# Kernel optimization log

Hardware: AMD Instinct MI355X
Metric: run time of the kernel (lower is better)

Reference implementation:

```python
import jax, jax.numpy as jnp
import numpy as np

D_MODEL = 1024
NUM_HEADS = 16
HEAD_DIM = D_MODEL // NUM_HEADS
D_FF = 4096
THETA = 10000.0
MAX_SEQ_LEN = 2048
EPS = 1e-5


def _init_linear(key, out_f, in_f):
    std = np.sqrt(2.0 / (out_f + in_f))
    w = jax.random.truncated_normal(key, -3.0, 3.0, (out_f, in_f), dtype=jnp.float32) * std
    return w


def setup_inputs() -> dict:
    key = jax.random.key(0)
    ks = jax.random.split(key, 9)
    x = jax.random.normal(ks[0], (4, 2048, D_MODEL), dtype=jnp.float32)
    return {
        "x": x,
        "wq": _init_linear(ks[1], D_MODEL, D_MODEL),
        "wk": _init_linear(ks[2], D_MODEL, D_MODEL),
        "wv": _init_linear(ks[3], D_MODEL, D_MODEL),
        "wo": _init_linear(ks[4], D_MODEL, D_MODEL),
        "ln1_w": jnp.ones((D_MODEL,), jnp.float32),
        "ln2_w": jnp.ones((D_MODEL,), jnp.float32),
        "up_w": _init_linear(ks[5], D_FF, D_MODEL),
        "gate_w": _init_linear(ks[6], D_FF, D_MODEL),
        "down_w": _init_linear(ks[7], D_MODEL, D_FF),
    }


def _rmsnorm(x, w):
    xf = x.astype(jnp.float32)
    inv_rms = jax.lax.rsqrt(jnp.mean(xf * xf, axis=-1, keepdims=True) + EPS)
    return (xf * inv_rms * w).astype(x.dtype)


def _rope_tables(seq_len):
    inv_freq = 1.0 / THETA ** (jnp.arange(0, HEAD_DIM, 2, dtype=jnp.float32) / HEAD_DIM)
    t = jnp.arange(seq_len, dtype=jnp.float32)
    freqs = jnp.outer(t, inv_freq)  # [s, hd/2]
    return jnp.cos(freqs), jnp.sin(freqs)


def _apply_rope(x, cos, sin):
    # x: [b, h, s, hd]; cos/sin: [s, hd/2] -> broadcast over b,h
    xe = x[..., 0::2]
    xo = x[..., 1::2]
    oe = xe * cos - xo * sin
    oo = xo * cos + xe * sin
    return jnp.stack((oe, oo), axis=-1).reshape(x.shape)


def reference(x, wq, wk, wv, wo, ln1_w, ln2_w, up_w, gate_w, down_w):
    b, s, d = x.shape
    h, hd = NUM_HEADS, HEAD_DIM

    # --- attention sublayer (pre-norm) ---
    xn = _rmsnorm(x, ln1_w)
    q = (xn @ wq.T).reshape(b, s, h, hd).transpose(0, 2, 1, 3)
    k = (xn @ wk.T).reshape(b, s, h, hd).transpose(0, 2, 1, 3)
    v = (xn @ wv.T).reshape(b, s, h, hd).transpose(0, 2, 1, 3)

    cos, sin = _rope_tables(s)
    q = _apply_rope(q, cos, sin)
    k = _apply_rope(k, cos, sin)

    scale = 1.0 / jnp.sqrt(jnp.float32(hd))
    logits = jnp.einsum("bhqd,bhkd->bhqk", q, k)
    causal = jnp.tril(jnp.ones((s, s), dtype=bool))
    logits = jnp.where(causal, logits, -jnp.inf)
    attn = jax.nn.softmax(logits * scale, axis=-1)
    ao = jnp.einsum("bhqk,bhkd->bhqd", attn, v)
    ao = ao.transpose(0, 2, 1, 3).reshape(b, s, d) @ wo.T
    x = x + ao

    # --- SwiGLU FFN sublayer (pre-norm) ---
    xn = _rmsnorm(x, ln2_w)
    up = xn @ up_w.T
    gate = xn @ gate_w.T
    ff = (up * jax.nn.sigmoid(up) * gate) @ down_w.T
    return x + ff
```

## Files before the change

### kernel.cpp

```cpp
#include <hip/hip_runtime.h>
#include <stdint.h>

#define SEQ   2048
#define NTOK  8192

typedef unsigned short u16;
typedef __bf16 bf16x8 __attribute__((ext_vector_type(8)));
typedef float  f32x4  __attribute__((ext_vector_type(4)));
typedef float  f32x16 __attribute__((ext_vector_type(16)));

__device__ __forceinline__ float b2f(u16 b) {
    union { unsigned u; float f; } v; v.u = ((unsigned)b) << 16; return v.f;
}
__device__ __forceinline__ u16 f2b(float f) {
    union { float f; unsigned u; } v; v.f = f;
    unsigned r = (v.u + 0x7fffu + ((v.u >> 16) & 1u)) >> 16;
    return (u16)r;
}
__device__ __forceinline__ u16 f2b_trunc(float f) {
    union { float f; unsigned u; } v; v.f = f;
    return (u16)(v.u >> 16);
}

__device__ __forceinline__ void gl_lds16(const void* g, void* l) {
    __builtin_amdgcn_global_load_lds(
        (const __attribute__((address_space(1))) void*)g,
        (__attribute__((address_space(3))) void*)l,
        16, 0, 0);
}

__global__ __launch_bounds__(256)
void cvt_all(const float* __restrict__ wq, const float* __restrict__ wk,
             const float* __restrict__ wv, const float* __restrict__ wo,
             const float* __restrict__ wup, const float* __restrict__ wgt,
             const float* __restrict__ wdn,
             u16* __restrict__ dq, u16* __restrict__ dk, u16* __restrict__ dv,
             u16* __restrict__ dw, u16* __restrict__ du, u16* __restrict__ dg,
             u16* __restrict__ dd)
{
    const int bid = blockIdx.x;
    const float* s; u16* d; int off;
    if (bid < 4096) {
        const int which = bid >> 10;
        off = (bid & 1023) * 256 + threadIdx.x;
        s = which == 0 ? wq : which == 1 ? wk : which == 2 ? wv : wo;
        d = which == 0 ? dq : which == 1 ? dk : which == 2 ? dv : dw;
    } else {
        const int which = (bid - 4096) >> 12;
        off = ((bid - 4096) & 4095) * 256 + threadIdx.x;
        s = which == 0 ? wup : which == 1 ? wgt : wdn;
        d = which == 0 ? du  : which == 1 ? dg  : dd;
    }
    float4 v = ((const float4*)s)[off];
    ushort4 o;
    o.x = f2b(v.x); o.y = f2b(v.y); o.z = f2b(v.z); o.w = f2b(v.w);
    ((ushort4*)d)[off] = o;
}

template<int EPI>
__global__ __launch_bounds__(256)
void gemm_bt(const u16* __restrict__ A, const u16* __restrict__ B,
             void* __restrict__ C, const void* __restrict__ E,
             int M, int N, int K, int ldc, int coff)
{
    __shared__ __align__(16) u16 As[128 * 64];
    __shared__ __align__(16) u16 Bs[128 * 64];

    const int tid  = threadIdx.x;
    const int lane = tid & 63;
    const int wid  = tid >> 6;
    const int m0 = blockIdx.y * 128;
    const int n0 = blockIdx.x * 128;
    const int wm = (wid >> 1) * 64;
    const int wn = (wid & 1) * 64;
    const int l31 = lane & 31, kg = lane >> 5;

    f32x16 acc[2][2];
#pragma unroll
    for (int i = 0; i < 2; i++)
#pragma unroll
        for (int j = 0; j < 2; j++)
#pragma unroll
            for (int r = 0; r < 16; r++) acc[i][j][r] = 0.f;

    const u16* Ag[4]; const u16* Bg[4]; u16* Al[4]; u16* Bl[4];
#pragma unroll
    for (int j = 0; j < 4; j++) {
        const int q = j * 256 + tid;
        const int r = q >> 3, s = q & 7, c = s ^ (r & 7);
        Ag[j] = A + (size_t)(m0 + r) * K + c * 8;
        Bg[j] = B + (size_t)(n0 + r) * K + c * 8;
        Al[j] = As + q * 8;
        Bl[j] = Bs + q * 8;
    }

    int arow[2], brow[2];
#pragma unroll
    for (int i = 0; i < 2; i++) { arow[i] = wm + i * 32 + l31; }
#pragma unroll
    for (int j = 0; j < 2; j++) { brow[j] = wn + j * 32 + l31; }

    for (int kt = 0; kt < K; kt += 64) {
        __syncthreads();
#pragma unroll
        for (int j = 0; j < 4; j++) {
            gl_lds16(Ag[j] + kt, Al[j]);
            gl_lds16(Bg[j] + kt, Bl[j]);
        }
        __syncthreads();

#pragma unroll
        for (int s = 0; s < 4; s++) {
            const int ch = s * 2 + kg;
            bf16x8 af[2], bf[2];
#pragma unroll
            for (int i = 0; i < 2; i++)
                af[i] = *(const bf16x8*)(
                    &As[arow[i] * 64 + ((ch ^ (arow[i] & 7)) * 8)]);
#pragma unroll
            for (int j = 0; j < 2; j++)
                bf[j] = *(const bf16x8*)(
                    &Bs[brow[j] * 64 + ((ch ^ (brow[j] & 7)) * 8)]);
#pragma unroll
            for (int i = 0; i < 2; i++)
#pragma unroll
                for (int j = 0; j < 2; j++)
                    acc[i][j] = __builtin_amdgcn_mfma_f32_32x32x16_bf16(
                        af[i], bf[j], acc[i][j], 0, 0, 0);
        }
    }

#pragma unroll
    for (int i = 0; i < 2; i++) {
#pragma unroll
        for (int r = 0; r < 16; r++) {
            const int row = m0 + wm + i * 32 + (r & 3) + 8 * (r >> 2) + 4 * kg;
#pragma unroll
            for (int j = 0; j < 2; j++) {
                const int col = n0 + wn + j * 32 + l31;
                const size_t idx = (size_t)row * ldc + coff + col;
                const float v = acc[i][j][r];
                if (EPI == 0) {
                    ((u16*)C)[idx] = f2b(v);
                } else {
                    ((float*)C)[idx] = v + ((const float*)E)[idx];
                }
            }
        }
    }
}

__global__ __launch_bounds__(256)
void gemm_mlp(const u16* __restrict__ A, const u16* __restrict__ Bg,
              const u16* __restrict__ Bu, u16* __restrict__ C, int K)
{
    __shared__ __align__(16) u16 As[128 * 64];
    __shared__ __align__(16) u16 Gs[64 * 64];
    __shared__ __align__(16) u16 Us[64 * 64];

    const int tid  = threadIdx.x;
    const int lane = tid & 63;
    const int wid  = tid >> 6;
    const int m0 = blockIdx.y * 128;
    const int n0 = blockIdx.x * 64;
    const int wm = (wid >> 1) * 64;
    const int wn = (wid & 1) * 32;
    const int l31 = lane & 31, kg = lane >> 5;

    f32x16 ag[2], au[2];
#pragma unroll
    for (int i = 0; i < 2; i++)
#pragma unroll
        for (int r = 0; r < 16; r++) { ag[i][r] = 0.f; au[i][r] = 0.f; }

    const u16* Ag[4]; u16* Al[4];
#pragma unroll
    for (int j = 0; j < 4; j++) {
        const int q = j * 256 + tid;
        const int r = q >> 3, s = q & 7, c = s ^ (r & 7);
        Ag[j] = A + (size_t)(m0 + r) * K + c * 8;
        Al[j] = As + q * 8;
    }
    const u16* Gg[2]; const u16* Ug[2]; u16* Gl[2]; u16* Ul[2];
#pragma unroll
    for (int j = 0; j < 2; j++) {
        const int q = j * 256 + tid;
        const int r = q >> 3, s = q & 7, c = s ^ (r & 7);
        Gg[j] = Bg + (size_t)(n0 + r) * K + c * 8;
        Ug[j] = Bu + (size_t)(n0 + r) * K + c * 8;
        Gl[j] = Gs + q * 8;
        Ul[j] = Us + q * 8;
    }

    int arow[2];
#pragma unroll
    for (int i = 0; i < 2; i++) arow[i] = wm + i * 32 + l31;
    const int brow = wn + l31;

    for (int kt = 0; kt < K; kt += 64) {
        __syncthreads();
#pragma unroll
        for (int j = 0; j < 4; j++) gl_lds16(Ag[j] + kt, Al[j]);
#pragma unroll
        for (int j = 0; j < 2; j++) {
            gl_lds16(Gg[j] + kt, Gl[j]);
            gl_lds16(Ug[j] + kt, Ul[j]);
        }
        __syncthreads();

#pragma unroll
        for (int s = 0; s < 4; s++) {
            const int ch = s * 2 + kg;
            bf16x8 af[2], gf, uf;
#pragma unroll
            for (int i = 0; i < 2; i++)
                af[i] = *(const bf16x8*)(
                    &As[arow[i] * 64 + ((ch ^ (arow[i] & 7)) * 8)]);
            gf = *(const bf16x8*)(&Gs[brow * 64 + ((ch ^ (brow & 7)) * 8)]);
            uf = *(const bf16x8*)(&Us[brow * 64 + ((ch ^ (brow & 7)) * 8)]);
#pragma unroll
            for (int i = 0; i < 2; i++) {
                ag[i] = __builtin_amdgcn_mfma_f32_32x32x16_bf16(
                    af[i], gf, ag[i], 0, 0, 0);
                au[i] = __builtin_amdgcn_mfma_f32_32x32x16_bf16(
                    af[i], uf, au[i], 0, 0, 0);
            }
        }
    }

#pragma unroll
    for (int i = 0; i < 2; i++) {
#pragma unroll
        for (int r = 0; r < 16; r++) {
            const int row = m0 + wm + i * 32 + (r & 3) + 8 * (r >> 2) + 4 * kg;
            const int col = n0 + wn + l31;
            const float u = au[i][r];
            const float g = ag[i][r];
            C[(size_t)row * 4096 + col] = f2b(u / (1.f + __expf(-u)) * g);
        }
    }
}

__global__ __launch_bounds__(256)
void rmsnorm_k(const float* __restrict__ xin, const float* __restrict__ w,
               u16* __restrict__ o)
{
    const int t = blockIdx.x;
    const int tid = threadIdx.x;
    float4 xv = ((const float4*)xin)[(size_t)t * 256 + tid];
    float ss = xv.x * xv.x + xv.y * xv.y + xv.z * xv.z + xv.w * xv.w;
#pragma unroll
    for (int off = 32; off > 0; off >>= 1) ss += __shfl_down(ss, off);
    __shared__ float red[4];
    const int lane = tid & 63, wv_ = tid >> 6;
    if (lane == 0) red[wv_] = ss;
    __syncthreads();
    const float tot = red[0] + red[1] + red[2] + red[3];
    const float inv = rsqrtf(tot * (1.f / 1024.f) + 1e-5f);
    float4 ww = ((const float4*)w)[tid];
    ushort4 ov;
    ov.x = f2b(xv.x * inv * ww.x);
    ov.y = f2b(xv.y * inv * ww.y);
    ov.z = f2b(xv.z * inv * ww.z);
    ov.w = f2b(xv.w * inv * ww.w);
    ((ushort4*)o)[(size_t)t * 256 + tid] = ov;
}

#define QSCALE 0.18033688011112042f

__global__ void rope_tab(float* __restrict__ cs, float* __restrict__ sn)
{
    const int s = blockIdx.x;
    const int i = threadIdx.x;
    const double inv = exp(-((double)(2 * i) / 64.0) * log(10000.0));
    const double ang = (double)s * inv;
    cs[s * 32 + i] = (float)cos(ang);
    sn[s * 32 + i] = (float)sin(ang);
}

__global__ __launch_bounds__(256)
void rope_apply(u16* __restrict__ qkv, const float* __restrict__ cs,
                const float* __restrict__ sn)
{
    const int t = blockIdx.x;
    const int s = t & (SEQ - 1);
    u16* row = qkv + (size_t)t * 3072;
    __shared__ float c_s[32], s_s[32];
    if (threadIdx.x < 32) {
        c_s[threadIdx.x] = cs[s * 32 + threadIdx.x];
        s_s[threadIdx.x] = sn[s * 32 + threadIdx.x];
    }
    __syncthreads();
#pragma unroll
    for (int rr = 0; rr < 2; rr++) {
        const int item = rr * 256 + threadIdx.x;
        const int hh = item >> 5, i = item & 31;
        const int f = hh * 64 + 2 * i;
        const float c = c_s[i], sv = s_s[i];
        float xe = b2f(row[f]), xo = b2f(row[f + 1]);
        row[f]     = f2b((xe * c - xo * sv) * QSCALE);
        row[f + 1] = f2b((xo * c + xe * sv) * QSCALE);
        xe = b2f(row[1024 + f]); xo = b2f(row[1024 + f + 1]);
        row[1024 + f]     = f2b(xe * c - xo * sv);
        row[1024 + f + 1] = f2b(xo * c + xe * sv);
    }
}

__global__ __launch_bounds__(256)
void vtrans(const u16* __restrict__ qkv, u16* __restrict__ vt)
{
    __shared__ u16 Ld[64 * 264];
    const int bh = blockIdx.x, st = blockIdx.y;
    const int b = bh >> 4, h = bh & 15;
    const int tid = threadIdx.x;
    const u16* src = qkv + ((size_t)(b * SEQ + st * 256 + tid)) * 3072 + 2048 + h * 64;
    uint4 v[8];
#pragma unroll
    for (int c = 0; c < 8; c++) v[c] = *(const uint4*)(src + c * 8);
#pragma unroll
    for (int c = 0; c < 8; c++) {
        const u16* pv = (const u16*)&v[c];
#pragma unroll
        for (int j = 0; j < 8; j++)
            Ld[(c * 8 + j) * 264 + tid] = pv[j];
    }
    __syncthreads();
    u16* dst = vt + (size_t)bh * (64 * SEQ) + st * 256;
#pragma unroll
    for (int cc = 0; cc < 8; cc++) {
        const int c = cc * 256 + tid;
        const int d = c >> 5, t8 = (c & 31) * 8;
        *(uint4*)(dst + (size_t)d * SEQ + t8) = *(const uint4*)(&Ld[d * 264 + t8]);
    }
}

__global__ __launch_bounds__(512)
void attn(const u16* __restrict__ qkv, const u16* __restrict__ vt,
          u16* __restrict__ ao)
{
    __shared__ __align__(16) u16 Ks[64 * 72];
    __shared__ __align__(16) u16 Vt[64 * 72];
    __shared__ __align__(16) u16 Ps[8][16 * 72];

    const int bh = blockIdx.x;
    const int qy = blockIdx.y;
    const int b = bh >> 4, h = bh & 15;
    const int tid = threadIdx.x, lane = tid & 63, wid = tid >> 6;
    const int am = lane & 15, grp = lane >> 4;
    const size_t tok0 = (size_t)b * SEQ;
    const u16* qbase = qkv + tok0 * 3072 + h * 64;
    const u16* kbase = qbase + 1024;
    const u16* vtg = vt + (size_t)bh * (64 * SEQ);

    union { uint4 u; bf16x8 b; } onesu;
    onesu.u = (uint4){0x3f803f80u, 0x3f803f80u, 0x3f803f80u, 0x3f803f80u};
    const bf16x8 ones = onesu.b;

    const int srow = tid >> 3, sc8 = (tid & 7) * 8;

#pragma unroll
    for (int tile = 0; tile < 2; tile++) {
        const int yt = tile == 0 ? qy : 15 - qy;
        const int qrow0 = yt * 128 + wid * 16;

        bf16x8 qf[2];
        {
            const u16* qp = qbase + (size_t)(qrow0 + am) * 3072 + grp * 8;
            qf[0] = *(const bf16x8*)(qp);
            qf[1] = *(const bf16x8*)(qp + 32);
        }

        f32x4 O[4], Ol;
#pragma unroll
        for (int j = 0; j < 4; j++) O[j] = (f32x4){0.f, 0.f, 0.f, 0.f};
        Ol = (f32x4){0.f, 0.f, 0.f, 0.f};

        const int ktend = yt * 128 + 64;
        for (int kt = 0; kt <= ktend; kt += 64) {
            __syncthreads();
            *(uint4*)(&Ks[srow * 72 + sc8]) =
                *(const uint4*)(kbase + (size_t)(kt + srow) * 3072 + sc8);
            *(uint4*)(&Vt[srow * 72 + sc8]) =
                *(const uint4*)(vtg + (size_t)srow * SEQ + kt + sc8);
            __syncthreads();

            if (kt > qrow0 + 15) continue;

            f32x4 st[4];
#pragma unroll
            for (int kk = 0; kk < 4; kk++) {
                const u16* kb = &Ks[(kk * 16 + am) * 72 + grp * 8];
                bf16x8 k0 = *(const bf16x8*)(kb);
                bf16x8 k1 = *(const bf16x8*)(kb + 32);
                f32x4 s = (f32x4){0.f, 0.f, 0.f, 0.f};
                s = __builtin_amdgcn_mfma_f32_16x16x32_bf16(qf[0], k0, s, 0, 0, 0);
                s = __builtin_amdgcn_mfma_f32_16x16x32_bf16(qf[1], k1, s, 0, 0, 0);
                st[kk] = s;
            }
            if (kt + 63 > qrow0) {
#pragma unroll
                for (int kk = 0; kk < 4; kk++) {
                    const int kg2 = kt + kk * 16 + am;
#pragma unroll
                    for (int r = 0; r < 4; r++) {
                        const int qg = qrow0 + grp * 4 + r;
                        if (kg2 > qg) st[kk][r] = -1e30f;
                    }
                }
            }
#pragma unroll
            for (int kk = 0; kk < 4; kk++)
#pragma unroll
                for (int r = 0; r < 4; r++)
                    st[kk][r] = exp2f(st[kk][r]);

            u16* pw = &Ps[wid][0];
#pragma unroll
            for (int kk = 0; kk < 4; kk++)
#pragma unroll
                for (int r = 0; r < 4; r++)
                    pw[(grp * 4 + r) * 72 + kk * 16 + am] = f2b_trunc(st[kk][r]);
            asm volatile("s_waitcnt lgkmcnt(0)" ::: "memory");

#pragma unroll
            for (int hh = 0; hh < 2; hh++) {
                bf16x8 pf = *(const bf16x8*)(&pw[am * 72 + hh * 32 + grp * 8]);
                Ol = __builtin_amdgcn_mfma_f32_16x16x32_bf16(pf, ones, Ol, 0, 0, 0);
#pragma unroll
                for (int jt = 0; jt < 4; jt++) {
                    bf16x8 vf = *(const bf16x8*)(
                        &Vt[(jt * 16 + am) * 72 + hh * 32 + grp * 8]);
                    O[jt] = __builtin_amdgcn_mfma_f32_16x16x32_bf16(
                        pf, vf, O[jt], 0, 0, 0);
                }
            }
        }

        u16* aorow = ao + (tok0 + qrow0) * 1024 + h * 64;
#pragma unroll
        for (int r = 0; r < 4; r++) {
            const int q = grp * 4 + r;
            const float invl = 1.f / Ol[r];
#pragma unroll
            for (int jt = 0; jt < 4; jt++)
                aorow[(size_t)q * 1024 + jt * 16 + am] = f2b(O[jt][r] * invl);
        }
    }
}

extern "C" void kernel_launch(void* const* d_in, const int* in_sizes, int n_in,
                              void* d_out, int out_size, void* d_ws, size_t ws_size,
                              hipStream_t stream)
{
    (void)in_sizes; (void)n_in; (void)out_size; (void)ws_size;
    const float* x     = (const float*)d_in[0];
    const float* wq    = (const float*)d_in[1];
    const float* wk    = (const float*)d_in[2];
    const float* wv    = (const float*)d_in[3];
    const float* wo    = (const float*)d_in[4];
    const float* ln1   = (const float*)d_in[5];
    const float* ln2   = (const float*)d_in[6];
    const float* wup   = (const float*)d_in[7];
    const float* wgate = (const float*)d_in[8];
    const float* wdown = (const float*)d_in[9];
    float* out = (float*)d_out;
    char* ws = (char*)d_ws;
    const size_t MB = 1024 * 1024;

    u16*   xn   = (u16*)(ws);
    u16*   ao   = (u16*)(ws);
    u16*   qkv  = (u16*)(ws + 16 * MB);
    u16*   hbuf = (u16*)(ws + 16 * MB);
    u16*   vtb  = (u16*)(ws + 64 * MB);
    float* x1   = (float*)(ws + 80 * MB);
    u16*   bwq  = (u16*)(ws + 112 * MB);
    u16*   bwk  = (u16*)(ws + 114 * MB);
    u16*   bwv  = (u16*)(ws + 116 * MB);
    u16*   bwo  = (u16*)(ws + 118 * MB);
    u16*   bwup = (u16*)(ws + 120 * MB);
    u16*   bwgt = (u16*)(ws + 128 * MB);
    u16*   bwdn = (u16*)(ws + 136 * MB);
    float* cst  = (float*)(ws + 144 * MB);
    float* snt  = (float*)(ws + 144 * MB + 262144);

    cvt_all<<<16384, 256, 0, stream>>>(wq, wk, wv, wo, wup, wgate, wdown,
                                       bwq, bwk, bwv, bwo, bwup, bwgt, bwdn);

    rope_tab<<<SEQ, 32, 0, stream>>>(cst, snt);
    rmsnorm_k<<<NTOK, 256, 0, stream>>>(x, ln1, xn);
    gemm_bt<0><<<dim3(24, 64), 256, 0, stream>>>(xn, bwq, qkv, nullptr, NTOK, 3072, 1024, 3072, 0);
    rope_apply<<<NTOK, 256, 0, stream>>>(qkv, cst, snt);
    vtrans<<<dim3(64, 8), 256, 0, stream>>>(qkv, vtb);
    attn<<<dim3(64, 8), 512, 0, stream>>>(qkv, vtb, ao);
    gemm_bt<1><<<dim3(8, 64), 256, 0, stream>>>(ao, bwo, x1, x, NTOK, 1024, 1024, 1024, 0);
    rmsnorm_k<<<NTOK, 256, 0, stream>>>(x1, ln2, xn);
    gemm_mlp<<<dim3(64, 64), 256, 0, stream>>>(xn, bwgt, bwup, hbuf, 1024);
    gemm_bt<1><<<dim3(8, 64), 256, 0, stream>>>(hbuf, bwdn, out, x1, NTOK, 1024, 4096, 1024, 0);
}
```

Baseline: 570.4 us.

## Rewrite gate/up MLP GEMM as 256x256 8-wave pipelined kernel with interleaved weights

Measured after the change: 565.8 us. No clear change (-0.8%).

```diff
diff --git a/kernel.cpp b/kernel.cpp
--- a/kernel.cpp
+++ b/kernel.cpp
@@ -35,26 +35,32 @@
              const float* __restrict__ wup, const float* __restrict__ wgt,
              const float* __restrict__ wdn,
              u16* __restrict__ dq, u16* __restrict__ dk, u16* __restrict__ dv,
-             u16* __restrict__ dw, u16* __restrict__ du, u16* __restrict__ dg,
-             u16* __restrict__ dd)
+             u16* __restrict__ dw, u16* __restrict__ dmu, u16* __restrict__ dd)
 {
     const int bid = blockIdx.x;
-    const float* s; u16* d; int off;
+    const float* s; u16* d; int osrc, odst;
     if (bid < 4096) {
         const int which = bid >> 10;
-        off = (bid & 1023) * 256 + threadIdx.x;
+        osrc = odst = (bid & 1023) * 256 + threadIdx.x;
         s = which == 0 ? wq : which == 1 ? wk : which == 2 ? wv : wo;
         d = which == 0 ? dq : which == 1 ? dk : which == 2 ? dv : dw;
     } else {
         const int which = (bid - 4096) >> 12;
-        off = ((bid - 4096) & 4095) * 256 + threadIdx.x;
-        s = which == 0 ? wup : which == 1 ? wgt : wdn;
-        d = which == 0 ? du  : which == 1 ? dg  : dd;
-    }
-    float4 v = ((const float4*)s)[off];
-    ushort4 o;
-    o.x = f2b(v.x); o.y = f2b(v.y); o.z = f2b(v.z); o.w = f2b(v.w);
-    ((ushort4*)d)[off] = o;
+        const int o = ((bid - 4096) & 4095) * 256 + threadIdx.x;
+        osrc = o;
+        if (which == 2) { s = wdn; d = dd; odst = o; }
+        else {
+            s = which == 0 ? wup : wgt;
+            d = dmu;
+            const int row = o >> 8;
+            const int rowp = ((row >> 4) << 5) + (row & 15) + (which == 0 ? 16 : 0);
+            odst = rowp * 256 + (o & 255);
+        }
+    }
+    float4 v = ((const float4*)s)[osrc];
+    ushort4 ov;
+    ov.x = f2b(v.x); ov.y = f2b(v.y); ov.z = f2b(v.z); ov.w = f2b(v.w);
+    ((ushort4*)d)[odst] = ov;
 }
 
 template<int EPI>
@@ -150,93 +156,158 @@
     }
 }
 
-__global__ __launch_bounds__(256)
-void gemm_mlp(const u16* __restrict__ A, const u16* __restrict__ Bg,
-              const u16* __restrict__ Bu, u16* __restrict__ C, int K)
-{
-    __shared__ __align__(16) u16 As[128 * 64];
-    __shared__ __align__(16) u16 Gs[64 * 64];
-    __shared__ __align__(16) u16 Us[64 * 64];
-
-    const int tid  = threadIdx.x;
-    const int lane = tid & 63;
-    const int wid  = tid >> 6;
-    const int m0 = blockIdx.y * 128;
-    const int n0 = blockIdx.x * 64;
-    const int wm = (wid >> 1) * 64;
-    const int wn = (wid & 1) * 32;
-    const int l31 = lane & 31, kg = lane >> 5;
-
-    f32x16 ag[2], au[2];
-#pragma unroll
-    for (int i = 0; i < 2; i++)
-#pragma unroll
-        for (int r = 0; r < 16; r++) { ag[i][r] = 0.f; au[i][r] = 0.f; }
-
-    const u16* Ag[4]; u16* Al[4];
-#pragma unroll
-    for (int j = 0; j < 4; j++) {
-        const int q = j * 256 + tid;
-        const int r = q >> 3, s = q & 7, c = s ^ (r & 7);
-        Ag[j] = A + (size_t)(m0 + r) * K + c * 8;
-        Al[j] = As + q * 8;
-    }
-    const u16* Gg[2]; const u16* Ug[2]; u16* Gl[2]; u16* Ul[2];
-#pragma unroll
-    for (int j = 0; j < 2; j++) {
-        const int q = j * 256 + tid;
-        const int r = q >> 3, s = q & 7, c = s ^ (r & 7);
-        Gg[j] = Bg + (size_t)(n0 + r) * K + c * 8;
-        Ug[j] = Bu + (size_t)(n0 + r) * K + c * 8;
-        Gl[j] = Gs + q * 8;
-        Ul[j] = Us + q * 8;
-    }
-
-    int arow[2];
-#pragma unroll
-    for (int i = 0; i < 2; i++) arow[i] = wm + i * 32 + l31;
-    const int brow = wn + l31;
-
-    for (int kt = 0; kt < K; kt += 64) {
-        __syncthreads();
-#pragma unroll
-        for (int j = 0; j < 4; j++) gl_lds16(Ag[j] + kt, Al[j]);
-#pragma unroll
-        for (int j = 0; j < 2; j++) {
-            gl_lds16(Gg[j] + kt, Gl[j]);
-            gl_lds16(Ug[j] + kt, Ul[j]);
-        }
-        __syncthreads();
-
-#pragma unroll
-        for (int s = 0; s < 4; s++) {
-            const int ch = s * 2 + kg;
-            bf16x8 af[2], gf, uf;
-#pragma unroll
-            for (int i = 0; i < 2; i++)
-                af[i] = *(const bf16x8*)(
-                    &As[arow[i] * 64 + ((ch ^ (arow[i] & 7)) * 8)]);
-            gf = *(const bf16x8*)(&Gs[brow * 64 + ((ch ^ (brow & 7)) * 8)]);
-            uf = *(const bf16x8*)(&Us[brow * 64 + ((ch ^ (brow & 7)) * 8)]);
-#pragma unroll
-            for (int i = 0; i < 2; i++) {
-                ag[i] = __builtin_amdgcn_mfma_f32_32x32x16_bf16(
-                    af[i], gf, ag[i], 0, 0, 0);
-                au[i] = __builtin_amdgcn_mfma_f32_32x32x16_bf16(
-                    af[i], uf, au[i], 0, 0, 0);
+#define MIDBAR \
+    __builtin_amdgcn_s_barrier(); \
+    asm volatile("s_waitcnt lgkmcnt(0)" ::: "memory"); \
+    __builtin_amdgcn_sched_barrier(0);
+
+#define PBAR \
+    __builtin_amdgcn_s_barrier(); \
+    asm volatile("" ::: "memory"); \
+    __builtin_amdgcn_sched_barrier(0);
+
+#define VMBAR4 \
+    asm volatile("s_waitcnt vmcnt(4)" ::: "memory"); \
+    __builtin_amdgcn_s_barrier(); \
+    asm volatile("" ::: "memory"); \
+    __builtin_amdgcn_sched_barrier(0);
+
+#define VMBAR0 \
+    asm volatile("s_waitcnt vmcnt(0)" ::: "memory"); \
+    __builtin_amdgcn_s_barrier(); \
+    asm volatile("" ::: "memory"); \
+    __builtin_amdgcn_sched_barrier(0);
+
+#define LDA(bufi, mh) { \
+    const u16* _ab = Ab##bufi + (mh) * 4096; \
+    _Pragma("unroll") \
+    for (int _m = 0; _m < 4; ++_m) { \
+        Aq[_m][0] = *(const bf16x8*)(_ab + _m * 1024 + axor0); \
+        Aq[_m][1] = *(const bf16x8*)(_ab + _m * 1024 + axor1); \
+    } }
+
+#define LDB(bufi, nh) { \
+    const u16* _bb = Bb##bufi + (nh) * 2048; \
+    _Pragma("unroll") \
+    for (int _n = 0; _n < 2; ++_n) { \
+        Bq[nh][_n][0] = *(const bf16x8*)(_bb + _n * 1024 + axor0); \
+        Bq[nh][_n][1] = *(const bf16x8*)(_bb + _n * 1024 + axor1); \
+    } }
+
+#define MM(mh, nh) \
+    __builtin_amdgcn_s_setprio(1); \
+    { _Pragma("unroll") \
+      for (int _m = 0; _m < 4; ++_m) { \
+        _Pragma("unroll") \
+        for (int _n = 0; _n < 2; ++_n) { \
+            acc[(mh)*4+_m][(nh)*2+_n] = __builtin_amdgcn_mfma_f32_16x16x32_bf16( \
+                Aq[_m][0], Bq[nh][_n][0], acc[(mh)*4+_m][(nh)*2+_n], 0, 0, 0); \
+            acc[(mh)*4+_m][(nh)*2+_n] = __builtin_amdgcn_mfma_f32_16x16x32_bf16( \
+                Aq[_m][1], Bq[nh][_n][1], acc[(mh)*4+_m][(nh)*2+_n], 0, 0, 0); \
+        } } } \
+    __builtin_amdgcn_s_setprio(0);
+
+#define STAGE_A(tile, half) { \
+    const u16* _s = pA0 + (size_t)(half) * 131072 + (size_t)(tile) * 64; \
+    u16* _d = lA0 + ((tile) & 1) * 16384 + (half) * 8192; \
+    gl_lds16(_s, _d); \
+    gl_lds16(_s + 65536, _d + 4096); }
+
+#define STAGE_B(tile, half) { \
+    const u16* _s = pB0 + (size_t)(half) * 131072 + (size_t)(tile) * 64; \
+    u16* _d = lB0 + ((tile) & 1) * 16384 + (half) * 8192; \
+    gl_lds16(_s, _d); \
+    gl_lds16(_s + 65536, _d + 4096); }
+
+__global__ __launch_bounds__(512, 2)
+void gemm8_mlp(const u16* __restrict__ A, const u16* __restrict__ Bc,
+               u16* __restrict__ H)
+{
+    __shared__ __align__(16) u16 As[32768];
+    __shared__ __align__(16) u16 Bs[32768];
+
+    const int tid = threadIdx.x, lane = tid & 63, wid = tid >> 6;
+    const int wr = wid >> 2, wc = wid & 3;
+    const int r15 = lane & 15, ks = lane >> 4;
+    const int m0 = blockIdx.y * 256, n0 = blockIdx.x * 256;
+
+    const int axor0 = ((ks) ^ (r15 & 7)) * 8;
+    const int axor1 = ((4 + ks) ^ (r15 & 7)) * 8;
+    const u16* Ab0 = As + wr * 8192 + r15 * 64;
+    const u16* Ab1 = As + 16384 + wr * 8192 + r15 * 64;
+    const u16* Bb0 = Bs + (wc >> 1) * 8192 + (wc & 1) * 4096 + r15 * 64;
+    const u16* Bb1 = Bs + 16384 + (wc >> 1) * 8192 + (wc & 1) * 4096 + r15 * 64;
+
+    const int r0 = tid >> 3, c0 = (tid & 7) ^ (r0 & 7);
+    const u16* pA0 = A  + (size_t)(m0 + r0) * 1024 + c0 * 8;
+    const u16* pB0 = Bc + (size_t)(n0 + r0) * 1024 + c0 * 8;
+    u16* lA0 = As + tid * 8;
+    u16* lB0 = Bs + tid * 8;
+
+    f32x4 acc[8][4];
+#pragma unroll
+    for (int m = 0; m < 8; ++m)
+#pragma unroll
+        for (int n = 0; n < 4; ++n)
+            acc[m][n] = (f32x4){0.f, 0.f, 0.f, 0.f};
+
+    bf16x8 Aq[4][2], Bq[2][2][2];
+
+    STAGE_A(0, 0); STAGE_A(0, 1);
+    STAGE_B(0, 0); STAGE_B(0, 1);
+    STAGE_B(1, 0); STAGE_B(1, 1);
+    asm volatile("s_waitcnt vmcnt(4)" ::: "memory");
+    __builtin_amdgcn_s_barrier();
+    asm volatile("" ::: "memory");
+    __builtin_amdgcn_sched_barrier(0);
+
+    for (int i = 0; i < 8; ++i) {
+        const int t1 = 2 * i + 1;
+        const int t2 = 2 * i + 2;
+        const int t3 = 2 * i + 3;
+        const bool st = (i < 7);
+
+        LDA(0, 0); LDB(0, 0);
+        STAGE_A(t1, 0);
+        MIDBAR; MM(0, 0); PBAR;
+        LDB(0, 1);
+        STAGE_A(t1, 1);
+        MIDBAR; MM(0, 1); PBAR;
+        LDA(0, 1);
+        if (st) STAGE_B(t2, 0);
+        MIDBAR; MM(1, 1); PBAR;
+        if (st) STAGE_B(t2, 1);
+        MIDBAR; MM(1, 0);
+        if (i == 7) { VMBAR0; } else { VMBAR4; }
+
+        LDA(1, 0); LDB(1, 0);
+        if (st) STAGE_A(t2, 0);
+        MIDBAR; MM(0, 0); PBAR;
+        LDB(1, 1);
+        if (st) STAGE_A(t2, 1);
+        MIDBAR; MM(0, 1); PBAR;
+        LDA(1, 1);
+        if (st) STAGE_B(t3, 0);
+        MIDBAR; MM(1, 1); PBAR;
+        if (st) STAGE_B(t3, 1);
+        MIDBAR; MM(1, 0);
+        VMBAR4;
+    }
+
+    const int orow0 = m0 + wr * 128;
+    const int ocol0 = (n0 >> 1) + wc * 32;
+#pragma unroll
+    for (int m = 0; m < 8; ++m) {
+#pragma unroll
+        for (int p = 0; p < 2; ++p) {
+#pragma unroll
+            for (int r = 0; r < 4; ++r) {
+                const int row = orow0 + m * 16 + ks * 4 + r;
+                const int col = ocol0 + p * 16 + r15;
+                const float g = acc[m][2 * p][r];
+                const float u = acc[m][2 * p + 1][r];
+                H[(size_t)row * 4096 + col] = f2b(u / (1.f + __expf(-u)) * g);
             }
-        }
-    }
-
-#pragma unroll
-    for (int i = 0; i < 2; i++) {
-#pragma unroll
-        for (int r = 0; r < 16; r++) {
-            const int row = m0 + wm + i * 32 + (r & 3) + 8 * (r >> 2) + 4 * kg;
-            const int col = n0 + wn + l31;
-            const float u = au[i][r];
-            const float g = ag[i][r];
-            C[(size_t)row * 4096 + col] = f2b(u / (1.f + __expf(-u)) * g);
         }
     }
 }
@@ -477,14 +548,13 @@
     u16*   bwk  = (u16*)(ws + 114 * MB);
     u16*   bwv  = (u16*)(ws + 116 * MB);
     u16*   bwo  = (u16*)(ws + 118 * MB);
-    u16*   bwup = (u16*)(ws + 120 * MB);
-    u16*   bwgt = (u16*)(ws + 128 * MB);
+    u16*   bwmu = (u16*)(ws + 120 * MB);
     u16*   bwdn = (u16*)(ws + 136 * MB);
     float* cst  = (float*)(ws + 144 * MB);
     float* snt  = (float*)(ws + 144 * MB + 262144);
 
     cvt_all<<<16384, 256, 0, stream>>>(wq, wk, wv, wo, wup, wgate, wdown,
-                                       bwq, bwk, bwv, bwo, bwup, bwgt, bwdn);
+                                       bwq, bwk, bwv, bwo, bwmu, bwdn);
 
     rope_tab<<<SEQ, 32, 0, stream>>>(cst, snt);
     rmsnorm_k<<<NTOK, 256, 0, stream>>>(x, ln1, xn);
@@ -494,6 +564,6 @@
     attn<<<dim3(64, 8), 512, 0, stream>>>(qkv, vtb, ao);
     gemm_bt<1><<<dim3(8, 64), 256, 0, stream>>>(ao, bwo, x1, x, NTOK, 1024, 1024, 1024, 0);
     rmsnorm_k<<<NTOK, 256, 0, stream>>>(x1, ln2, xn);
-    gemm_mlp<<<dim3(64, 64), 256, 0, stream>>>(xn, bwgt, bwup, hbuf, 1024);
+    gemm8_mlp<<<dim3(32, 32), 512, 0, stream>>>(xn, bwmu, hbuf);
     gemm_bt<1><<<dim3(8, 64), 256, 0, stream>>>(hbuf, bwdn, out, x1, NTOK, 1024, 4096, 1024, 0);
 }
```
